# Kernel tuning notes

Hardware: AMD Instinct MI355X
Metric: run time of the kernel (lower is better)

The kernel has to match this reference:

```python
import jax, jax.numpy as jnp
import numpy as np

NEG_SLOPE = 0.2  # DenseGATConv default negative_slope


def dense_gat(x, adj, W, att_src, att_dst, bias):
    # x: [B,N,Cin], adj: [B,N,N] (self-loops already added), W: [Cin,H*C]
    B, N, _ = x.shape
    H, C = att_src.shape
    h = (x @ W).reshape(B, N, H, C)
    a_src = jnp.einsum('bnhc,hc->bnh', h, att_src)  # [B,N,H]
    a_dst = jnp.einsum('bnhc,hc->bnh', h, att_dst)
    # alpha[b,i,j,h] = a_src[b,j,h] + a_dst[b,i,h]  (softmax over j, axis=2)
    alpha = a_src[:, None, :, :] + a_dst[:, :, None, :]
    alpha = jnp.where(alpha >= 0, alpha, NEG_SLOPE * alpha)  # leaky_relu
    mask = (adj != 0)[..., None]  # [B,N,N,1]
    alpha = jax.nn.softmax(jnp.where(mask, alpha, -1e30), axis=2)
    out = jnp.einsum('bijh,bjhc->bihc', alpha, h).reshape(B, N, H * C)
    return out + bias


def setup_inputs() -> dict:
    key = jax.random.key(0)
    ks = jax.random.split(key, 8)
    B, N, D = 1, 8192, 128
    x = jax.random.normal(ks[0], (B, N, D), dtype=jnp.float32)
    adj = (jax.random.uniform(ks[1], (B, N, N)) < 0.01).astype(jnp.float32)
    idx = jnp.arange(N)
    adj = adj.at[:, idx, idx].set(1.0)  # DenseGATConv add_loop=True
    s = 1.0 / np.sqrt(D)
    lin = lambda k: jax.random.uniform(k, (D, D), minval=-s, maxval=s, dtype=jnp.float32)
    att = lambda k: jax.random.normal(k, (1, D), dtype=jnp.float32) * 0.1  # heads=1
    return dict(
        x=x, adj=adj,
        W0=lin(ks[2]), att_src0=att(ks[3]), att_dst0=att(ks[4]), b0=jnp.zeros((D,), jnp.float32),
        W1=lin(ks[5]), att_src1=att(ks[6]), att_dst1=att(ks[7]), b1=jnp.zeros((D,), jnp.float32),
    )


def reference(x, adj, W0, att_src0, att_dst0, b0, W1, att_src1, att_dst1, b1):
    out0 = dense_gat(x, adj, W0, att_src0, att_dst0, b0)
    out0 = jax.nn.relu(out0)  # relu_layers_index = [0]
    out1 = dense_gat(out0, adj, W1, att_src1, att_dst1, b1)
    # dropout_rate = 0 -> dropout is identity; squeeze batch dim as in block
    return (out0[0], out1[0])
```

## Files before the change

kernel.cpp:

```cpp
#include <hip/hip_runtime.h>

#define MAXDEG 192
#define NEG_SLOPE 0.2f
#define D 128

__device__ __forceinline__ float bf2f(unsigned short u) {
    return __uint_as_float(((unsigned)u) << 16);
}
__device__ __forceinline__ unsigned short f2bf(float f) {
    unsigned u = __float_as_uint(f);
    return (unsigned short)((u + 0x7fffu + ((u >> 16) & 1u)) >> 16);
}
__device__ __forceinline__ unsigned pack2bf(float x, float y) {
    return (unsigned)f2bf(x) | ((unsigned)f2bf(y) << 16);
}
__device__ __forceinline__ int is_f32(const void* adj) {
    return ((const unsigned*)adj)[0] == 0x3F800000u;
}

__device__ __forceinline__ void ell_group(
        int g, const void* __restrict__ adj, int N, int f32m,
        unsigned short* __restrict__ cols, int* __restrict__ deg,
        int* __restrict__ cnt ) {
    const int w = threadIdx.x >> 6, lane = threadIdx.x & 63;
    const int row = g * 4 + w;
    if (lane == 0) cnt[w] = 0;
    __syncthreads();
    unsigned short* crow = cols + (size_t)row * MAXDEG;
    if (f32m) {
        const float4* arow = (const float4*)((const float*)adj + (size_t)row * N);
        const int nv = N / 4;
        for (int v = lane; v < nv; v += 128) {
            float4 u0 = arow[v];
            float4 u1 = arow[v + 64];
            const unsigned* a0 = (const unsigned*)&u0;
            const unsigned* a1 = (const unsigned*)&u1;
            #pragma unroll
            for (int e = 0; e < 4; e++)
                if (a0[e]) { int p = atomicAdd(&cnt[w], 1); if (p < MAXDEG) crow[p] = (unsigned short)(v * 4 + e); }
            #pragma unroll
            for (int e = 0; e < 4; e++)
                if (a1[e]) { int p = atomicAdd(&cnt[w], 1); if (p < MAXDEG) crow[p] = (unsigned short)((v + 64) * 4 + e); }
        }
    } else {
        const uint4* arow = (const uint4*)((const unsigned short*)adj + (size_t)row * N);
        const int nv = N / 8;
        for (int v = lane; v < nv; v += 128) {
            uint4 u0 = arow[v];
            uint4 u1 = arow[v + 64];
            const unsigned short* s0 = (const unsigned short*)&u0;
            const unsigned short* s1 = (const unsigned short*)&u1;
            #pragma unroll
            for (int e = 0; e < 8; e++)
                if (s0[e]) { int p = atomicAdd(&cnt[w], 1); if (p < MAXDEG) crow[p] = (unsigned short)(v * 8 + e); }
            #pragma unroll
            for (int e = 0; e < 8; e++)
                if (s1[e]) { int p = atomicAdd(&cnt[w], 1); if (p < MAXDEG) crow[p] = (unsigned short)((v + 64) * 8 + e); }
        }
    }
    __syncthreads();
    if (lane == 0) deg[row] = cnt[w] < MAXDEG ? cnt[w] : MAXDEG;
}

__device__ __forceinline__ void gemm_tile32(
        int t, const void* __restrict__ A, const void* __restrict__ W,
        int aF, int f32m, const void* __restrict__ attS, const void* __restrict__ attD,
        unsigned short* __restrict__ Hb, float* __restrict__ asrc, float* __restrict__ adst,
        float* __restrict__ smem) {
    float* xs = smem;
    float* ws = smem + 4096;
    const int tid = threadIdx.x;
    const size_t row0 = (size_t)t * 32;

    if (aF) {
        const float4* av = (const float4*)((const float*)A + row0 * D);
        float4* xl = (float4*)xs;
        #pragma unroll
        for (int k = 0; k < 4; k++) xl[tid + 256 * k] = av[tid + 256 * k];
    } else {
        const uint4* av = (const uint4*)((const unsigned short*)A + row0 * D);
        #pragma unroll
        for (int k = 0; k < 2; k++) {
            uint4 u = av[tid + 256 * k];
            const unsigned short* us = (const unsigned short*)&u;
            #pragma unroll
            for (int e = 0; e < 8; e++) xs[(tid + 256 * k) * 8 + e] = bf2f(us[e]);
        }
    }

    const int tx = tid & 31, ty = tid >> 5;
    const int c0 = tx * 4, r0 = ty * 4;
    float acc[4][4] = {};
    for (int p = 0; p < 4; p++) {
        __syncthreads();
        if (f32m) {
            const float4* wv = (const float4*)((const float*)W + (size_t)p * 32 * D);
            float4* wl = (float4*)ws;
            #pragma unroll
            for (int k = 0; k < 4; k++) wl[tid + 256 * k] = wv[tid + 256 * k];
        } else {
            const uint4* wv = (const uint4*)((const unsigned short*)W + (size_t)p * 32 * D);
            #pragma unroll
            for (int k = 0; k < 2; k++) {
                uint4 u = wv[tid + 256 * k];
                const unsigned short* us = (const unsigned short*)&u;
                #pragma unroll
                for (int e = 0; e < 8; e++) ws[(tid + 256 * k) * 8 + e] = bf2f(us[e]);
            }
        }
        __syncthreads();
        #pragma unroll 8
        for (int k = 0; k < 32; k++) {
            float4 wv = *(const float4*)&ws[k * D + c0];
            #pragma unroll
            for (int i = 0; i < 4; i++) {
                float xv = xs[(r0 + i) * D + p * 32 + k];
                acc[i][0] += xv * wv.x; acc[i][1] += xv * wv.y;
                acc[i][2] += xv * wv.z; acc[i][3] += xv * wv.w;
            }
        }
    }
    #pragma unroll
    for (int i = 0; i < 4; i++) {
        ushort4 hv;
        hv.x = f2bf(acc[i][0]); hv.y = f2bf(acc[i][1]);
        hv.z = f2bf(acc[i][2]); hv.w = f2bf(acc[i][3]);
        *(ushort4*)&Hb[(row0 + r0 + i) * D + c0] = hv;
    }

    float aSv[4], aDv[4];
    #pragma unroll
    for (int j = 0; j < 4; j++) {
        aSv[j] = f32m ? ((const float*)attS)[c0 + j] : bf2f(((const unsigned short*)attS)[c0 + j]);
        aDv[j] = f32m ? ((const float*)attD)[c0 + j] : bf2f(((const unsigned short*)attD)[c0 + j]);
    }
    #pragma unroll
    for (int i = 0; i < 4; i++) {
        float s = acc[i][0] * aSv[0] + acc[i][1] * aSv[1] + acc[i][2] * aSv[2] + acc[i][3] * aSv[3];
        float d = acc[i][0] * aDv[0] + acc[i][1] * aDv[1] + acc[i][2] * aDv[2] + acc[i][3] * aDv[3];
        #pragma unroll
        for (int off = 16; off > 0; off >>= 1) {
            s += __shfl_down(s, off, 32);
            d += __shfl_down(d, off, 32);
        }
        if (tx == 0) {
            asrc[row0 + r0 + i] = s;
            adst[row0 + r0 + i] = d;
        }
    }
}

__device__ __forceinline__ float2 agg_row_bf(
        int row, const unsigned short* __restrict__ Hb,
        const float* __restrict__ asrc, float ai,
        const unsigned short* __restrict__ crow, int d,
        const void* __restrict__ bias, int f32m, int relu,
        float* __restrict__ scn, unsigned short* __restrict__ sjj, int lane) {
    const int s0 = lane, s1 = lane + 64, s2 = lane + 128;
    unsigned short j0 = 0, j1 = 0, j2 = 0;
    float e0 = -3e38f, e1 = -3e38f, e2 = -3e38f;
    if (s0 < d) { j0 = crow[s0]; float e = asrc[j0] + ai; e0 = (e >= 0.f) ? e : NEG_SLOPE * e; }
    if (s1 < d) { j1 = crow[s1]; float e = asrc[j1] + ai; e1 = (e >= 0.f) ? e : NEG_SLOPE * e; }
    if (s2 < d) { j2 = crow[s2]; float e = asrc[j2] + ai; e2 = (e >= 0.f) ? e : NEG_SLOPE * e; }
    float m = fmaxf(e0, fmaxf(e1, e2));
    #pragma unroll
    for (int off = 1; off < 64; off <<= 1) m = fmaxf(m, __shfl_xor(m, off));
    float p0 = (s0 < d) ? __expf(e0 - m) : 0.f;
    float p1 = (s1 < d) ? __expf(e1 - m) : 0.f;
    float p2 = (s2 < d) ? __expf(e2 - m) : 0.f;
    float l = p0 + p1 + p2;
    #pragma unroll
    for (int off = 1; off < 64; off <<= 1) l += __shfl_xor(l, off);
    const float invl = 1.f / l;
    scn[s0] = p0 * invl; sjj[s0] = j0;
    scn[s1] = p1 * invl; sjj[s1] = j1;
    scn[s2] = p2 * invl; sjj[s2] = j2;

    const unsigned* H2 = (const unsigned*)Hb;
    float ax[8], ay[8];
    #pragma unroll
    for (int u = 0; u < 8; u++) { ax[u] = 0.f; ay[u] = 0.f; }
    int k = 0;
    for (; k + 7 < d; k += 8) {
        int jj[8]; float ww[8]; unsigned vv[8];
        #pragma unroll
        for (int u = 0; u < 8; u++) { jj[u] = sjj[k + u]; ww[u] = scn[k + u]; }
        #pragma unroll
        for (int u = 0; u < 8; u++) vv[u] = H2[(size_t)jj[u] * 64 + lane];
        #pragma unroll
        for (int u = 0; u < 8; u++) {
            ax[u] += ww[u] * bf2f((unsigned short)(vv[u] & 0xffff));
            ay[u] += ww[u] * bf2f((unsigned short)(vv[u] >> 16));
        }
    }
    for (; k < d; k++) {
        const int j = sjj[k];
        const float wk = scn[k];
        unsigned v = H2[(size_t)j * 64 + lane];
        ax[0] += wk * bf2f((unsigned short)(v & 0xffff));
        ay[0] += wk * bf2f((unsigned short)(v >> 16));
    }
    #pragma unroll
    for (int u = 1; u < 8; u++) { ax[0] += ax[u]; ay[0] += ay[u]; }

    const int c0 = lane * 2;
    const float bx = f32m ? ((const float*)bias)[c0]     : bf2f(((const unsigned short*)bias)[c0]);
    const float by = f32m ? ((const float*)bias)[c0 + 1] : bf2f(((const unsigned short*)bias)[c0 + 1]);
    float vx = ax[0] + bx, vy = ay[0] + by;
    if (relu) { vx = fmaxf(vx, 0.f); vy = fmaxf(vy, 0.f); }
    return make_float2(vx, vy);
}

__global__ __launch_bounds__(256) void ell_gemm0(
        const void* __restrict__ x, const void* __restrict__ adj,
        const void* __restrict__ W0, const void* __restrict__ aS0,
        const void* __restrict__ aD0, int N,
        unsigned short* __restrict__ cols, int* __restrict__ deg,
        unsigned short* __restrict__ h, float* __restrict__ asrc, float* __restrict__ adst) {
    __shared__ float smem[8192];
    const int bid = blockIdx.x;
    const int f32m = is_f32(adj);
    const int GT = N / 32;
    if (bid < GT)
        gemm_tile32(bid, x, W0, f32m, f32m, aS0, aD0, h, asrc, adst, smem);
    else
        ell_group(bid - GT, adj, N, f32m, cols, deg, (int*)smem);
}

__global__ __launch_bounds__(256) void agg0_gemm1(
        const unsigned short* __restrict__ h,
        const float* __restrict__ asrc0, const float* __restrict__ adst0,
        const unsigned short* __restrict__ cols, const int* __restrict__ deg,
        const void* __restrict__ b0, const void* __restrict__ W1,
        const void* __restrict__ aS1, const void* __restrict__ aD1,
        const void* __restrict__ adjFlag, void* __restrict__ out,
        unsigned short* __restrict__ h2,
        float* __restrict__ asrc1, float* __restrict__ adst1, int N) {
    __shared__ float xs[8 * D];
    __shared__ float wstage[32 * D];
    __shared__ float scnA[4 * MAXDEG];
    __shared__ unsigned short sjjA[4 * MAXDEG];
    const int tid = threadIdx.x;
    const int w = tid >> 6, lane = tid & 63;
    const int f32m = is_f32(adjFlag);

    #pragma unroll
    for (int pass = 0; pass < 2; pass++) {
        const int rl = pass * 4 + w;
        const int row = blockIdx.x * 8 + rl;
        float2 v = agg_row_bf(row, h, asrc0, adst0[row],
                              cols + (size_t)row * MAXDEG, deg[row],
                              b0, f32m, 1,
                              scnA + w * MAXDEG, sjjA + w * MAXDEG, lane);
        xs[rl * D + 2 * lane]     = v.x;
        xs[rl * D + 2 * lane + 1] = v.y;
        if (f32m) ((float2*)out)[(size_t)row * 64 + lane] = v;
        else      ((unsigned*)out)[(size_t)row * 64 + lane] = pack2bf(v.x, v.y);
    }

    const int tx = tid & 31, ty = tid >> 5;
    const int c0 = tx * 4;
    float acc[4] = {};
    for (int p = 0; p < 4; p++) {
        __syncthreads();
        if (f32m) {
            const float4* wv = (const float4*)((const float*)W1 + (size_t)p * 32 * D);
            float4* wl = (float4*)wstage;
            #pragma unroll
            for (int k = 0; k < 4; k++) wl[tid + 256 * k] = wv[tid + 256 * k];
        } else {
            const uint4* wv = (const uint4*)((const unsigned short*)W1 + (size_t)p * 32 * D);
            #pragma unroll
            for (int k = 0; k < 2; k++) {
                uint4 u = wv[tid + 256 * k];
                const unsigned short* us = (const unsigned short*)&u;
                #pragma unroll
                for (int e = 0; e < 8; e++) wstage[(tid + 256 * k) * 8 + e] = bf2f(us[e]);
            }
        }
        __syncthreads();
        #pragma unroll 8
        for (int k = 0; k < 32; k++) {
            float4 wv = *(const float4*)&wstage[k * D + c0];
            float xv = xs[ty * D + p * 32 + k];
            acc[0] += xv * wv.x; acc[1] += xv * wv.y;
            acc[2] += xv * wv.z; acc[3] += xv * wv.w;
        }
    }
    const size_t row1 = (size_t)blockIdx.x * 8 + ty;
    ushort4 hv;
    hv.x = f2bf(acc[0]); hv.y = f2bf(acc[1]); hv.z = f2bf(acc[2]); hv.w = f2bf(acc[3]);
    *(ushort4*)&h2[row1 * D + c0] = hv;

    float aSv[4], aDv[4];
    #pragma unroll
    for (int j = 0; j < 4; j++) {
        aSv[j] = f32m ? ((const float*)aS1)[c0 + j] : bf2f(((const unsigned short*)aS1)[c0 + j]);
        aDv[j] = f32m ? ((const float*)aD1)[c0 + j] : bf2f(((const unsigned short*)aD1)[c0 + j]);
    }
    float s = acc[0] * aSv[0] + acc[1] * aSv[1] + acc[2] * aSv[2] + acc[3] * aSv[3];
    float d = acc[0] * aDv[0] + acc[1] * aDv[1] + acc[2] * aDv[2] + acc[3] * aDv[3];
    #pragma unroll
    for (int off = 16; off > 0; off >>= 1) {
        s += __shfl_down(s, off, 32);
        d += __shfl_down(d, off, 32);
    }
    if (tx == 0) {
        asrc1[row1] = s;
        adst1[row1] = d;
    }
}

__global__ __launch_bounds__(256) void aggregate1(
        const unsigned short* __restrict__ h2,
        const float* __restrict__ asrc1, const float* __restrict__ adst1,
        const unsigned short* __restrict__ cols, const int* __restrict__ deg,
        const void* __restrict__ b1, const void* __restrict__ adjFlag,
        void* __restrict__ out, int N) {
    __shared__ float scnA[4 * MAXDEG];
    __shared__ unsigned short sjjA[4 * MAXDEG];
    const int w = threadIdx.x >> 6, lane = threadIdx.x & 63;
    const int row = blockIdx.x * 4 + w;
    const int f32m = is_f32(adjFlag);
    float2 v = agg_row_bf(row, h2, asrc1, adst1[row],
                          cols + (size_t)row * MAXDEG, deg[row],
                          b1, f32m, 0,
                          scnA + w * MAXDEG, sjjA + w * MAXDEG, lane);
    const size_t off2 = (size_t)N * 64;
    if (f32m) ((float2*)out)[off2 + (size_t)row * 64 + lane] = v;
    else      ((unsigned*)out)[off2 + (size_t)row * 64 + lane] = pack2bf(v.x, v.y);
}

extern "C" void kernel_launch(void* const* d_in, const int* in_sizes, int n_in,
                              void* d_out, int out_size, void* d_ws, size_t ws_size,
                              hipStream_t stream) {
    const int N = in_sizes[0] / D;

    char* w = (char*)d_ws;
    int* deg             = (int*)w;            w += (size_t)N * sizeof(int);
    unsigned short* cols = (unsigned short*)w; w += (size_t)N * MAXDEG * sizeof(unsigned short);
    unsigned short* h    = (unsigned short*)w; w += (size_t)N * D * sizeof(unsigned short);
    unsigned short* h2   = (unsigned short*)w; w += (size_t)N * D * sizeof(unsigned short);
    float* asrc0         = (float*)w;          w += (size_t)N * sizeof(float);
    float* adst0         = (float*)w;          w += (size_t)N * sizeof(float);
    float* asrc1         = (float*)w;          w += (size_t)N * sizeof(float);
    float* adst1         = (float*)w;

    const void* adj = d_in[1];

    ell_gemm0<<<N / 32 + N / 4, 256, 0, stream>>>(
        d_in[0], adj, d_in[2], d_in[3], d_in[4], N, cols, deg, h, asrc0, adst0);

    agg0_gemm1<<<N / 8, 256, 0, stream>>>(
        h, asrc0, adst0, cols, deg, d_in[5], d_in[6], d_in[7], d_in[8],
        adj, d_out, h2, asrc1, adst1, N);

    aggregate1<<<N / 4, 256, 0, stream>>>(
        h2, asrc1, adst1, cols, deg, d_in[9], adj, d_out, N);
}
```

Measured before the change: 419.1 us.

## Fuse three GAT stages into one persistent cooperative kernel with grid syncs

Replaces the three separate launches with a single cooperative persistent kernel that runs the first GEMM tiles, then ELL construction, then layer-0 aggregation fused with the second GEMM, then layer-1 aggregation, separated by grid.sync. The ELL row groups are handed out through an atomic work queue so blocks balance the scan over the dense adjacency. The aim is to remove launch gaps and tail effects between stages. In exchange it adds a memset, an occupancy query and grid-wide barriers, and the grid is capped at 1024 blocks, which may limit parallelism in the memory-bound adjacency scan.

```diff
diff --git a/kernel.cpp b/kernel.cpp
--- a/kernel.cpp
+++ b/kernel.cpp
@@ -1,4 +1,7 @@
 #include <hip/hip_runtime.h>
+#include <hip/hip_cooperative_groups.h>
+
+namespace cg = cooperative_groups;
 
 #define MAXDEG 192
 #define NEG_SLOPE 0.2f
@@ -211,6 +214,146 @@
     return make_float2(vx, vy);
 }
 
+__device__ __forceinline__ void agg0_gemm1_body(
+        int q, const unsigned short* __restrict__ h,
+        const float* __restrict__ asrc0, const float* __restrict__ adst0,
+        const unsigned short* __restrict__ cols, const int* __restrict__ deg,
+        const void* __restrict__ b0, const void* __restrict__ W1,
+        const void* __restrict__ aS1, const void* __restrict__ aD1, int f32m,
+        void* __restrict__ out, unsigned short* __restrict__ h2,
+        float* __restrict__ asrc1, float* __restrict__ adst1,
+        float* __restrict__ xs8, float* __restrict__ wst,
+        float* __restrict__ scnA, unsigned short* __restrict__ sjjA) {
+    const int tid = threadIdx.x;
+    const int w = tid >> 6, lane = tid & 63;
+
+    #pragma unroll
+    for (int pass = 0; pass < 2; pass++) {
+        const int rl = pass * 4 + w;
+        const int row = q * 8 + rl;
+        float2 v = agg_row_bf(row, h, asrc0, adst0[row],
+                              cols + (size_t)row * MAXDEG, deg[row],
+                              b0, f32m, 1,
+                              scnA + w * MAXDEG, sjjA + w * MAXDEG, lane);
+        xs8[rl * D + 2 * lane]     = v.x;
+        xs8[rl * D + 2 * lane + 1] = v.y;
+        if (f32m) ((float2*)out)[(size_t)row * 64 + lane] = v;
+        else      ((unsigned*)out)[(size_t)row * 64 + lane] = pack2bf(v.x, v.y);
+    }
+
+    const int tx = tid & 31, ty = tid >> 5;
+    const int c0 = tx * 4;
+    float acc[4] = {};
+    for (int p = 0; p < 4; p++) {
+        __syncthreads();
+        if (f32m) {
+            const float4* wv = (const float4*)((const float*)W1 + (size_t)p * 32 * D);
+            float4* wl = (float4*)wst;
+            #pragma unroll
+            for (int k = 0; k < 4; k++) wl[tid + 256 * k] = wv[tid + 256 * k];
+        } else {
+            const uint4* wv = (const uint4*)((const unsigned short*)W1 + (size_t)p * 32 * D);
+            #pragma unroll
+            for (int k = 0; k < 2; k++) {
+                uint4 u = wv[tid + 256 * k];
+                const unsigned short* us = (const unsigned short*)&u;
+                #pragma unroll
+                for (int e = 0; e < 8; e++) wst[(tid + 256 * k) * 8 + e] = bf2f(us[e]);
+            }
+        }
+        __syncthreads();
+        #pragma unroll 8
+        for (int k = 0; k < 32; k++) {
+            float4 wv = *(const float4*)&wst[k * D + c0];
+            float xv = xs8[ty * D + p * 32 + k];
+            acc[0] += xv * wv.x; acc[1] += xv * wv.y;
+            acc[2] += xv * wv.z; acc[3] += xv * wv.w;
+        }
+    }
+    const size_t row1 = (size_t)q * 8 + ty;
+    ushort4 hv;
+    hv.x = f2bf(acc[0]); hv.y = f2bf(acc[1]); hv.z = f2bf(acc[2]); hv.w = f2bf(acc[3]);
+    *(ushort4*)&h2[row1 * D + c0] = hv;
+
+    float aSv[4], aDv[4];
+    #pragma unroll
+    for (int j = 0; j < 4; j++) {
+        aSv[j] = f32m ? ((const float*)aS1)[c0 + j] : bf2f(((const unsigned short*)aS1)[c0 + j]);
+        aDv[j] = f32m ? ((const float*)aD1)[c0 + j] : bf2f(((const unsigned short*)aD1)[c0 + j]);
+    }
+    float s = acc[0] * aSv[0] + acc[1] * aSv[1] + acc[2] * aSv[2] + acc[3] * aSv[3];
+    float d = acc[0] * aDv[0] + acc[1] * aDv[1] + acc[2] * aDv[2] + acc[3] * aDv[3];
+    #pragma unroll
+    for (int off = 16; off > 0; off >>= 1) {
+        s += __shfl_down(s, off, 32);
+        d += __shfl_down(d, off, 32);
+    }
+    if (tx == 0) {
+        asrc1[row1] = s;
+        adst1[row1] = d;
+    }
+}
+
+__global__ __launch_bounds__(256) void gat_coop(
+        const void* __restrict__ x, const void* __restrict__ adj,
+        const void* __restrict__ W0, const void* __restrict__ aS0,
+        const void* __restrict__ aD0, const void* __restrict__ b0,
+        const void* __restrict__ W1, const void* __restrict__ aS1,
+        const void* __restrict__ aD1, const void* __restrict__ b1,
+        void* __restrict__ out, int N,
+        int* __restrict__ qhead, int* __restrict__ deg,
+        unsigned short* __restrict__ cols,
+        unsigned short* __restrict__ h, unsigned short* __restrict__ h2,
+        float* __restrict__ asrc0, float* __restrict__ adst0,
+        float* __restrict__ asrc1, float* __restrict__ adst1) {
+    cg::grid_group grid = cg::this_grid();
+    __shared__ __align__(16) char smemRaw[32768];
+    __shared__ int sgrp;
+    float* smemF = (float*)smemRaw;
+    float* xs8   = (float*)smemRaw;
+    float* wst   = (float*)(smemRaw + 4096);
+    float* scnA  = (float*)(smemRaw + 20480);
+    unsigned short* sjjA = (unsigned short*)(smemRaw + 23552);
+    const int G = gridDim.x;
+    const int f32m = is_f32(adj);
+    const int GT = N / 32, NG = N / 4;
+
+    for (int t = blockIdx.x; t < GT; t += G) {
+        __syncthreads();
+        gemm_tile32(t, x, W0, f32m, f32m, aS0, aD0, h, asrc0, adst0, smemF);
+    }
+    __syncthreads();
+    for (;;) {
+        if (threadIdx.x == 0) sgrp = atomicAdd(qhead, 1);
+        __syncthreads();
+        const int g = sgrp;
+        if (g >= NG) break;
+        ell_group(g, adj, N, f32m, cols, deg, (int*)smemRaw);
+    }
+    __threadfence();
+    grid.sync();
+
+    for (int q = blockIdx.x; q < N / 8; q += G) {
+        __syncthreads();
+        agg0_gemm1_body(q, h, asrc0, adst0, cols, deg, b0, W1, aS1, aD1, f32m,
+                        out, h2, asrc1, adst1, xs8, wst, scnA, sjjA);
+    }
+    __threadfence();
+    grid.sync();
+
+    const int w = threadIdx.x >> 6, lane = threadIdx.x & 63;
+    for (int q = blockIdx.x; q < N / 4; q += G) {
+        const int row = q * 4 + w;
+        float2 v = agg_row_bf(row, h2, asrc1, adst1[row],
+                              cols + (size_t)row * MAXDEG, deg[row],
+                              b1, f32m, 0,
+                              scnA + w * MAXDEG, sjjA + w * MAXDEG, lane);
+        const size_t off2 = (size_t)N * 64;
+        if (f32m) ((float2*)out)[off2 + (size_t)row * 64 + lane] = v;
+        else      ((unsigned*)out)[off2 + (size_t)row * 64 + lane] = pack2bf(v.x, v.y);
+    }
+}
+
 __global__ __launch_bounds__(256) void ell_gemm0(
         const void* __restrict__ x, const void* __restrict__ adj,
         const void* __restrict__ W0, const void* __restrict__ aS0,
@@ -236,79 +379,13 @@
         const void* __restrict__ adjFlag, void* __restrict__ out,
         unsigned short* __restrict__ h2,
         float* __restrict__ asrc1, float* __restrict__ adst1, int N) {
-    __shared__ float xs[8 * D];
-    __shared__ float wstage[32 * D];
+    __shared__ float xs8[8 * D];
+    __shared__ float wst[32 * D];
     __shared__ float scnA[4 * MAXDEG];
     __shared__ unsigned short sjjA[4 * MAXDEG];
-    const int tid = threadIdx.x;
-    const int w = tid >> 6, lane = tid & 63;
     const int f32m = is_f32(adjFlag);
-
-    #pragma unroll
-    for (int pass = 0; pass < 2; pass++) {
-        const int rl = pass * 4 + w;
-        const int row = blockIdx.x * 8 + rl;
-        float2 v = agg_row_bf(row, h, asrc0, adst0[row],
-                              cols + (size_t)row * MAXDEG, deg[row],
-                              b0, f32m, 1,
-                              scnA + w * MAXDEG, sjjA + w * MAXDEG, lane);
-        xs[rl * D + 2 * lane]     = v.x;
-        xs[rl * D + 2 * lane + 1] = v.y;
-        if (f32m) ((float2*)out)[(size_t)row * 64 + lane] = v;
-        else      ((unsigned*)out)[(size_t)row * 64 + lane] = pack2bf(v.x, v.y);
-    }
-
-    const int tx = tid & 31, ty = tid >> 5;
-    const int c0 = tx * 4;
-    float acc[4] = {};
-    for (int p = 0; p < 4; p++) {
-        __syncthreads();
-        if (f32m) {
-            const float4* wv = (const float4*)((const float*)W1 + (size_t)p * 32 * D);
-            float4* wl = (float4*)wstage;
-            #pragma unroll
-            for (int k = 0; k < 4; k++) wl[tid + 256 * k] = wv[tid + 256 * k];
-        } else {
-            const uint4* wv = (const uint4*)((const unsigned short*)W1 + (size_t)p * 32 * D);
-            #pragma unroll
-            for (int k = 0; k < 2; k++) {
-                uint4 u = wv[tid + 256 * k];
-                const unsigned short* us = (const unsigned short*)&u;
-                #pragma unroll
-                for (int e = 0; e < 8; e++) wstage[(tid + 256 * k) * 8 + e] = bf2f(us[e]);
-            }
-        }
-        __syncthreads();
-        #pragma unroll 8
-        for (int k = 0; k < 32; k++) {
-            float4 wv = *(const float4*)&wstage[k * D + c0];
-            float xv = xs[ty * D + p * 32 + k];
-            acc[0] += xv * wv.x; acc[1] += xv * wv.y;
-            acc[2] += xv * wv.z; acc[3] += xv * wv.w;
-        }
-    }
-    const size_t row1 = (size_t)blockIdx.x * 8 + ty;
-    ushort4 hv;
-    hv.x = f2bf(acc[0]); hv.y = f2bf(acc[1]); hv.z = f2bf(acc[2]); hv.w = f2bf(acc[3]);
-    *(ushort4*)&h2[row1 * D + c0] = hv;
-
-    float aSv[4], aDv[4];
-    #pragma unroll
-    for (int j = 0; j < 4; j++) {
-        aSv[j] = f32m ? ((const float*)aS1)[c0 + j] : bf2f(((const unsigned short*)aS1)[c0 + j]);
-        aDv[j] = f32m ? ((const float*)aD1)[c0 + j] : bf2f(((const unsigned short*)aD1)[c0 + j]);
-    }
-    float s = acc[0] * aSv[0] + acc[1] * aSv[1] + acc[2] * aSv[2] + acc[3] * aSv[3];
-    float d = acc[0] * aDv[0] + acc[1] * aDv[1] + acc[2] * aDv[2] + acc[3] * aDv[3];
-    #pragma unroll
-    for (int off = 16; off > 0; off >>= 1) {
-        s += __shfl_down(s, off, 32);
-        d += __shfl_down(d, off, 32);
-    }
-    if (tx == 0) {
-        asrc1[row1] = s;
-        adst1[row1] = d;
-    }
+    agg0_gemm1_body(blockIdx.x, h, asrc0, adst0, cols, deg, b0, W1, aS1, aD1,
+                    f32m, out, h2, asrc1, adst1, xs8, wst, scnA, sjjA);
 }
 
 __global__ __launch_bounds__(256) void aggregate1(
@@ -337,6 +414,7 @@
     const int N = in_sizes[0] / D;
 
     char* w = (char*)d_ws;
+    int* qhead           = (int*)w;            w += 256;
     int* deg             = (int*)w;            w += (size_t)N * sizeof(int);
     unsigned short* cols = (unsigned short*)w; w += (size_t)N * MAXDEG * sizeof(unsigned short);
     unsigned short* h    = (unsigned short*)w; w += (size_t)N * D * sizeof(unsigned short);
@@ -348,13 +426,37 @@
 
     const void* adj = d_in[1];
 
-    ell_gemm0<<<N / 32 + N / 4, 256, 0, stream>>>(
-        d_in[0], adj, d_in[2], d_in[3], d_in[4], N, cols, deg, h, asrc0, adst0);
-
-    agg0_gemm1<<<N / 8, 256, 0, stream>>>(
-        h, asrc0, adst0, cols, deg, d_in[5], d_in[6], d_in[7], d_in[8],
-        adj, d_out, h2, asrc1, adst1, N);
-
-    aggregate1<<<N / 4, 256, 0, stream>>>(
-        h2, asrc1, adst1, cols, deg, d_in[9], adj, d_out, N);
-}
+    hipMemsetAsync(qhead, 0, 64, stream);
+
+    int bpc = 0;
+    hipError_t qe = hipOccupancyMaxActiveBlocksPerMultiprocessor(&bpc, gat_coop, 256, 0);
+    int G = (qe == hipSuccess && bpc > 0) ? bpc * 256 : 512;
+    if (G > 1024) G = 1024;
+
+    const void* a_x = d_in[0];
+    const void* a_W0 = d_in[2]; const void* a_aS0 = d_in[3];
+    const void* a_aD0 = d_in[4]; const void* a_b0 = d_in[5];
+    const void* a_W1 = d_in[6]; const void* a_aS1 = d_in[7];
+    const void* a_aD1 = d_in[8]; const void* a_b1 = d_in[9];
+    void* a_out = d_out; int a_N = N;
+    void* args[] = {
+        (void*)&a_x, (void*)&adj, (void*)&a_W0, (void*)&a_aS0, (void*)&a_aD0,
+        (void*)&a_b0, (void*)&a_W1, (void*)&a_aS1, (void*)&a_aD1, (void*)&a_b1,
+        (void*)&a_out, (void*)&a_N, (void*)&qhead, (void*)&deg, (void*)&cols,
+        (void*)&h, (void*)&h2, (void*)&asrc0, (void*)&adst0,
+        (void*)&asrc1, (void*)&adst1
+    };
+
+    hipError_t ce = hipLaunchCooperativeKernel(
+        reinterpret_cast<void*>(gat_coop), dim3(G), dim3(256), args, 0, stream);
+
+    if (ce != hipSuccess) {
+        ell_gemm0<<<N / 32 + N / 4, 256, 0, stream>>>(
+            d_in[0], adj, d_in[2], d_in[3], d_in[4], N, cols, deg, h, asrc0, adst0);
+        agg0_gemm1<<<N / 8, 256, 0, stream>>>(
+            h, asrc0, adst0, cols, deg, d_in[5], d_in[6], d_in[7], d_in[8],
+            adj, d_out, h2, asrc1, adst1, N);
+        aggregate1<<<N / 4, 256, 0, stream>>>(
+            h2, asrc1, adst1, cols, deg, d_in[9], adj, d_out, N);
+    }
+}
```

After: 680.6 us. 1.62x slower.

## Deepen adjacency scan loads, shrink GEMM W staging, reorder ELL/GEMM blocks

Applied to the files above, without the earlier changes.

The ELL build loop now issues four 16-byte loads per lane per iteration instead of two, giving more memory-level parallelism while streaming the dense adjacency. The bf16 path checks 32-bit words before testing individual halves, so all-zero pairs are skipped cheaply. The layer-0 GEMM stages W in 16-row chunks, which cuts shared memory from 32KB to 24KB per block to allow more resident blocks, at the cost of twice as many barriers. ELL blocks are now dispatched before GEMM blocks so the bandwidth-heavy scan starts first.

```diff
diff --git a/kernel.cpp b/kernel.cpp
--- a/kernel.cpp
+++ b/kernel.cpp
@@ -16,6 +16,25 @@
 }
 __device__ __forceinline__ int is_f32(const void* adj) {
     return ((const unsigned*)adj)[0] == 0x3F800000u;
+}
+
+__device__ __forceinline__ void ell_scan_u4_bf16(
+        uint4 u, int base, int* cnt, unsigned short* crow) {
+    const unsigned* a = (const unsigned*)&u;
+    #pragma unroll
+    for (int e = 0; e < 4; e++) {
+        unsigned wv = a[e];
+        if (wv) {
+            if (wv & 0xffffu) {
+                int p = atomicAdd(cnt, 1);
+                if (p < MAXDEG) crow[p] = (unsigned short)(base + 2 * e);
+            }
+            if (wv >> 16) {
+                int p = atomicAdd(cnt, 1);
+                if (p < MAXDEG) crow[p] = (unsigned short)(base + 2 * e + 1);
+            }
+        }
+    }
 }
 
 __device__ __forceinline__ void ell_group(
@@ -30,32 +49,33 @@
     if (f32m) {
         const float4* arow = (const float4*)((const float*)adj + (size_t)row * N);
         const int nv = N / 4;
-        for (int v = lane; v < nv; v += 128) {
+        for (int v = lane; v < nv; v += 256) {
             float4 u0 = arow[v];
             float4 u1 = arow[v + 64];
-            const unsigned* a0 = (const unsigned*)&u0;
-            const unsigned* a1 = (const unsigned*)&u1;
-            #pragma unroll
-            for (int e = 0; e < 4; e++)
-                if (a0[e]) { int p = atomicAdd(&cnt[w], 1); if (p < MAXDEG) crow[p] = (unsigned short)(v * 4 + e); }
-            #pragma unroll
-            for (int e = 0; e < 4; e++)
-                if (a1[e]) { int p = atomicAdd(&cnt[w], 1); if (p < MAXDEG) crow[p] = (unsigned short)((v + 64) * 4 + e); }
+            float4 u2 = arow[v + 128];
+            float4 u3 = arow[v + 192];
+            const float4* us[4] = {&u0, &u1, &u2, &u3};
+            #pragma unroll
+            for (int q = 0; q < 4; q++) {
+                const unsigned* a = (const unsigned*)us[q];
+                const int base = (v + 64 * q) * 4;
+                #pragma unroll
+                for (int e = 0; e < 4; e++)
+                    if (a[e]) { int p = atomicAdd(&cnt[w], 1); if (p < MAXDEG) crow[p] = (unsigned short)(base + e); }
+            }
         }
     } else {
         const uint4* arow = (const uint4*)((const unsigned short*)adj + (size_t)row * N);
         const int nv = N / 8;
-        for (int v = lane; v < nv; v += 128) {
+        for (int v = lane; v < nv; v += 256) {
             uint4 u0 = arow[v];
             uint4 u1 = arow[v + 64];
-            const unsigned short* s0 = (const unsigned short*)&u0;
-            const unsigned short* s1 = (const unsigned short*)&u1;
-            #pragma unroll
-            for (int e = 0; e < 8; e++)
-                if (s0[e]) { int p = atomicAdd(&cnt[w], 1); if (p < MAXDEG) crow[p] = (unsigned short)(v * 8 + e); }
-            #pragma unroll
-            for (int e = 0; e < 8; e++)
-                if (s1[e]) { int p = atomicAdd(&cnt[w], 1); if (p < MAXDEG) crow[p] = (unsigned short)((v + 64) * 8 + e); }
+            uint4 u2 = arow[v + 128];
+            uint4 u3 = arow[v + 192];
+            ell_scan_u4_bf16(u0, (v)       * 8, &cnt[w], crow);
+            ell_scan_u4_bf16(u1, (v + 64)  * 8, &cnt[w], crow);
+            ell_scan_u4_bf16(u2, (v + 128) * 8, &cnt[w], crow);
+            ell_scan_u4_bf16(u3, (v + 192) * 8, &cnt[w], crow);
         }
     }
     __syncthreads();
@@ -91,30 +111,26 @@
     const int tx = tid & 31, ty = tid >> 5;
     const int c0 = tx * 4, r0 = ty * 4;
     float acc[4][4] = {};
-    for (int p = 0; p < 4; p++) {
+    for (int p = 0; p < 8; p++) {
         __syncthreads();
         if (f32m) {
-            const float4* wv = (const float4*)((const float*)W + (size_t)p * 32 * D);
+            const float4* wv = (const float4*)((const float*)W + (size_t)p * 16 * D);
             float4* wl = (float4*)ws;
             #pragma unroll
-            for (int k = 0; k < 4; k++) wl[tid + 256 * k] = wv[tid + 256 * k];
+            for (int k = 0; k < 2; k++) wl[tid + 256 * k] = wv[tid + 256 * k];
         } else {
-            const uint4* wv = (const uint4*)((const unsigned short*)W + (size_t)p * 32 * D);
-            #pragma unroll
-            for (int k = 0; k < 2; k++) {
-                uint4 u = wv[tid + 256 * k];
-                const unsigned short* us = (const unsigned short*)&u;
-                #pragma unroll
-                for (int e = 0; e < 8; e++) ws[(tid + 256 * k) * 8 + e] = bf2f(us[e]);
-            }
+            uint4 u = ((const uint4*)((const unsigned short*)W + (size_t)p * 16 * D))[tid];
+            const unsigned short* us = (const unsigned short*)&u;
+            #pragma unroll
+            for (int e = 0; e < 8; e++) ws[tid * 8 + e] = bf2f(us[e]);
         }
         __syncthreads();
         #pragma unroll 8
-        for (int k = 0; k < 32; k++) {
+        for (int k = 0; k < 16; k++) {
             float4 wv = *(const float4*)&ws[k * D + c0];
             #pragma unroll
             for (int i = 0; i < 4; i++) {
-                float xv = xs[(r0 + i) * D + p * 32 + k];
+                float xv = xs[(r0 + i) * D + p * 16 + k];
                 acc[i][0] += xv * wv.x; acc[i][1] += xv * wv.y;
                 acc[i][2] += xv * wv.z; acc[i][3] += xv * wv.w;
             }
@@ -217,14 +233,14 @@
         const void* __restrict__ aD0, int N,
         unsigned short* __restrict__ cols, int* __restrict__ deg,
         unsigned short* __restrict__ h, float* __restrict__ asrc, float* __restrict__ adst) {
-    __shared__ float smem[8192];
+    __shared__ float smem[6144];
     const int bid = blockIdx.x;
     const int f32m = is_f32(adj);
-    const int GT = N / 32;
-    if (bid < GT)
-        gemm_tile32(bid, x, W0, f32m, f32m, aS0, aD0, h, asrc, adst, smem);
+    const int NG = N / 4;
+    if (bid < NG)
+        ell_group(bid, adj, N, f32m, cols, deg, (int*)smem);
     else
-        ell_group(bid - GT, adj, N, f32m, cols, deg, (int*)smem);
+        gemm_tile32(bid - NG, x, W0, f32m, f32m, aS0, aD0, h, asrc, adst, smem);
 }
 
 __global__ __launch_bounds__(256) void agg0_gemm1(
@@ -236,24 +252,25 @@
         const void* __restrict__ adjFlag, void* __restrict__ out,
         unsigned short* __restrict__ h2,
         float* __restrict__ asrc1, float* __restrict__ adst1, int N) {
-    __shared__ float xs[8 * D];
-    __shared__ float wstage[32 * D];
+    __shared__ float xs8[8 * D];
+    __shared__ float wst[32 * D];
     __shared__ float scnA[4 * MAXDEG];
     __shared__ unsigned short sjjA[4 * MAXDEG];
     const int tid = threadIdx.x;
     const int w = tid >> 6, lane = tid & 63;
     const int f32m = is_f32(adjFlag);
+    const int q = blockIdx.x;
 
     #pragma unroll
     for (int pass = 0; pass < 2; pass++) {
         const int rl = pass * 4 + w;
-        const int row = blockIdx.x * 8 + rl;
+        const int row = q * 8 + rl;
         float2 v = agg_row_bf(row, h, asrc0, adst0[row],
                               cols + (size_t)row * MAXDEG, deg[row],
                               b0, f32m, 1,
                               scnA + w * MAXDEG, sjjA + w * MAXDEG, lane);
-        xs[rl * D + 2 * lane]     = v.x;
-        xs[rl * D + 2 * lane + 1] = v.y;
+        xs8[rl * D + 2 * lane]     = v.x;
+        xs8[rl * D + 2 * lane + 1] = v.y;
         if (f32m) ((float2*)out)[(size_t)row * 64 + lane] = v;
         else      ((unsigned*)out)[(size_t)row * 64 + lane] = pack2bf(v.x, v.y);
     }
@@ -265,7 +282,7 @@
         __syncthreads();
         if (f32m) {
             const float4* wv = (const float4*)((const float*)W1 + (size_t)p * 32 * D);
-            float4* wl = (float4*)wstage;
+            float4* wl = (float4*)wst;
             #pragma unroll
             for (int k = 0; k < 4; k++) wl[tid + 256 * k] = wv[tid + 256 * k];
         } else {
@@ -275,19 +292,19 @@
                 uint4 u = wv[tid + 256 * k];
                 const unsigned short* us = (const unsigned short*)&u;
                 #pragma unroll
-                for (int e = 0; e < 8; e++) wstage[(tid + 256 * k) * 8 + e] = bf2f(us[e]);
+                for (int e = 0; e < 8; e++) wst[(tid + 256 * k) * 8 + e] = bf2f(us[e]);
             }
         }
         __syncthreads();
         #pragma unroll 8
         for (int k = 0; k < 32; k++) {
-            float4 wv = *(const float4*)&wstage[k * D + c0];
-            float xv = xs[ty * D + p * 32 + k];
+            float4 wv = *(const float4*)&wst[k * D + c0];
+            float xv = xs8[ty * D + p * 32 + k];
             acc[0] += xv * wv.x; acc[1] += xv * wv.y;
             acc[2] += xv * wv.z; acc[3] += xv * wv.w;
         }
     }
-    const size_t row1 = (size_t)blockIdx.x * 8 + ty;
+    const size_t row1 = (size_t)q * 8 + ty;
     ushort4 hv;
     hv.x = f2bf(acc[0]); hv.y = f2bf(acc[1]); hv.z = f2bf(acc[2]); hv.w = f2bf(acc[3]);
     *(ushort4*)&h2[row1 * D + c0] = hv;
@@ -348,7 +365,7 @@
 
     const void* adj = d_in[1];
 
-    ell_gemm0<<<N / 32 + N / 4, 256, 0, stream>>>(
+    ell_gemm0<<<N / 4 + N / 32, 256, 0, stream>>>(
         d_in[0], adj, d_in[2], d_in[3], d_in[4], N, cols, deg, h, asrc0, adst0);
 
     agg0_gemm1<<<N / 8, 256, 0, stream>>>(
```

After: 428.2 us. 2.2% more time.
